# Kernel optimization log

Hardware: AMD Instinct MI355X
Metric: run time of the kernel (lower is better)

Reference implementation:

```python
import jax, jax.numpy as jnp
import numpy as np

PC_RANGE = (-54.0, -54.0, -5.0, 54.0, 54.0, 3.0)
VOXEL = (0.075, 0.075, 0.2)
STRIDE = 8
FW = 180  # feature map size along x
FH = 180  # feature map size along y
NUM_CLASS = 2
M = 500   # num_max_objs
MIN_RADIUS = 2
OVERLAP = 0.1
C_IN = 128
HM_C = 2
REG_C = 9
B = 4


def conv2d(x, w, b=None):
    y = jax.lax.conv_general_dilated(x, w, (1, 1), 'SAME',
                                     dimension_numbers=('NCHW', 'OIHW', 'NCHW'))
    return y if b is None else y + b[None, :, None, None]


def bn(x, g, b, m, v, eps=1e-5):
    inv = g / jnp.sqrt(v + eps)
    return x * inv[None, :, None, None] + (b - m * inv)[None, :, None, None]


def gaussian_radius(height, width, min_overlap):
    # centernet_utils.gaussian_radius
    b1 = height + width
    c1 = width * height * (1.0 - min_overlap) / (1.0 + min_overlap)
    r1 = (b1 + jnp.sqrt(jnp.maximum(b1 * b1 - 4.0 * c1, 0.0))) / 2.0
    b2 = 2.0 * (height + width)
    c2 = (1.0 - min_overlap) * width * height
    r2 = (b2 + jnp.sqrt(jnp.maximum(b2 * b2 - 16.0 * c2, 0.0))) / 2.0
    a3 = 4.0 * min_overlap
    b3 = -2.0 * min_overlap * (height + width)
    c3 = (min_overlap - 1.0) * width * height
    r3 = (b3 + jnp.sqrt(jnp.maximum(b3 * b3 - 4.0 * a3 * c3, 0.0))) / (2.0 * a3)
    return jnp.minimum(jnp.minimum(r1, r2), r3)


def assign_targets(gt):
    # gt: (B, M, 8) = [x, y, z, dx, dy, dz, ry, cls]; cls==0 / zero box = padding
    x, y, z = gt[..., 0], gt[..., 1], gt[..., 2]
    dx, dy, dz, ry = gt[..., 3], gt[..., 4], gt[..., 5], gt[..., 6]
    cls = gt[..., 7].astype(jnp.int32)
    coord_x = jnp.clip((x - PC_RANGE[0]) / VOXEL[0] / STRIDE, 0.0, FW - 0.5)
    coord_y = jnp.clip((y - PC_RANGE[1]) / VOXEL[1] / STRIDE, 0.0, FH - 0.5)
    cxi = coord_x.astype(jnp.int32)
    cyi = coord_y.astype(jnp.int32)
    dxp = dx / VOXEL[0] / STRIDE
    dyp = dy / VOXEL[1] / STRIDE
    radius = jnp.maximum(gaussian_radius(dxp, dyp, OVERLAP).astype(jnp.int32), MIN_RADIUS)
    valid = (dxp > 0) & (dyp > 0)
    pos = valid & (cls >= 1)

    # --- dense gaussian splat, max-reduced per class (= draw_gaussian_to_heatmap) ---
    ddx = jnp.arange(FW)[None, None, :] - cxi[..., None]   # (B,M,FW)
    ddy = jnp.arange(FH)[None, None, :] - cyi[..., None]   # (B,M,FH)
    sigma = (2.0 * radius.astype(jnp.float32) + 1.0) / 6.0
    d2 = (ddy[..., :, None] ** 2 + ddx[..., None, :] ** 2).astype(jnp.float32)  # (B,M,FH,FW)
    g = jnp.exp(-d2 / (2.0 * sigma[..., None, None] ** 2))
    win = (jnp.abs(ddy) <= radius[..., None])[..., :, None] & \
          (jnp.abs(ddx) <= radius[..., None])[..., None, :]
    g = jnp.where(win & pos[..., None, None], g, 0.0)
    seg = jnp.where(pos, cls - 1, NUM_CLASS)
    hmv = jax.vmap(lambda gv, sv: jax.ops.segment_max(gv, sv, num_segments=NUM_CLASS + 1))(
        g.reshape(B, M, FH * FW), seg)
    heatmap = jnp.maximum(hmv[:, :NUM_CLASS].reshape(B, NUM_CLASS, FH, FW), 0.0)
    heatmap_mask = (heatmap > 0).astype(gt.dtype)

    # --- inds / mask / ret_boxes (5 slots per object: center + 4 neighbors) ---
    base_ind = cyi * FW + cxi
    w_cond = VOXEL[0] * STRIDE > dy / 4.0   # faithful: uses temp_w = gt[:,4]
    l_cond = VOXEL[1] * STRIDE > dx / 4.0   # faithful: uses temp_l = gt[:,3]
    left = cxi - 1 >= 0
    right = cxi + 1 < FW
    up = cyi - 1 >= 0
    down = cyi + 1 < FH
    m0 = jnp.where(valid, jnp.where(cls >= 1, 1, -1), 0)
    s1 = valid & ~w_cond & left
    s2 = valid & ~w_cond & right
    s3 = valid & ~l_cond & up
    s4 = valid & ~l_cond & down
    mask = jnp.stack([m0,
                      jnp.where(s1, m0, 0), jnp.where(s2, m0, 0),
                      jnp.where(s3, m0, 0), jnp.where(s4, m0, 0)], -1).reshape(B, 5 * M)
    inds = jnp.stack([jnp.where(valid, base_ind, 0),
                      jnp.where(s1, base_ind - 1, 0), jnp.where(s2, base_ind + 1, 0),
                      jnp.where(s3, base_ind - FW, 0), jnp.where(s4, base_ind + FW, 0)],
                     -1).reshape(B, 5 * M).astype(jnp.int32)
    offx = coord_x - cxi.astype(gt.dtype)
    offy = coord_y - cyi.astype(gt.dtype)
    base = jnp.stack([offx, offy, z,
                      jnp.log(jnp.maximum(dx, 1e-8)),
                      jnp.log(jnp.maximum(dy, 1e-8)),
                      jnp.log(jnp.maximum(dz, 1e-8)),
                      jnp.cos(ry), jnp.sin(ry)], -1)          # (B,M,8)
    z5 = jnp.zeros((B, M), gt.dtype)
    dx_adj = jnp.stack([z5, s1.astype(gt.dtype), -s2.astype(gt.dtype), z5, z5], -1)  # (B,M,5)
    dy_adj = jnp.stack([z5, z5, z5, s3.astype(gt.dtype), -s4.astype(gt.dtype)], -1)
    zero5 = jnp.zeros_like(dx_adj)
    delta = jnp.stack([dx_adj, dy_adj, zero5, zero5, zero5, zero5, zero5, zero5], -1)  # (B,M,5,8)
    rb = (base[:, :, None, :] + delta) * valid[:, :, None, None].astype(gt.dtype)
    ret_boxes = rb.reshape(B, 5 * M, 8)
    return heatmap, ret_boxes, inds, mask, heatmap_mask


def setup_inputs():
    key = jax.random.key(0)
    ks = jax.random.split(key, 12)
    x = jax.random.normal(ks[0], (B, C_IN, FH, FW), jnp.float32)
    # realistic gt boxes; last 150 per scene are zero padding
    cxy = jax.random.uniform(ks[1], (B, M, 2), minval=-50.0, maxval=50.0)
    zc = jax.random.uniform(ks[2], (B, M, 1), minval=-2.0, maxval=1.0)
    dims = jax.random.uniform(ks[3], (B, M, 3), minval=0.5, maxval=6.0)
    ry = jax.random.uniform(ks[4], (B, M, 1), minval=-3.14, maxval=3.14)
    cls = jax.random.randint(ks[5], (B, M, 1), 1, NUM_CLASS + 1).astype(jnp.float32)
    vm = (jnp.arange(M) < 350)[None, :, None].astype(jnp.float32)
    gt_boxes = jnp.concatenate([cxy, zc, dims, ry, cls], -1) * vm
    p = lambda k, s, sc: jax.random.normal(k, s, jnp.float32) * sc
    return {
        'x': x, 'gt_boxes': gt_boxes,
        'conv1_w': p(ks[6], (C_IN, C_IN, 3, 3), 0.02),
        'bn1_g': jnp.ones((C_IN,)), 'bn1_b': jnp.zeros((C_IN,)),
        'bn1_m': jnp.zeros((C_IN,)), 'bn1_v': jnp.ones((C_IN,)),
        'conv2_w': p(ks[7], (C_IN, C_IN, 3, 3), 0.02),
        'bn2_g': jnp.ones((C_IN,)), 'bn2_b': jnp.zeros((C_IN,)),
        'bn2_m': jnp.zeros((C_IN,)), 'bn2_v': jnp.ones((C_IN,)),
        'hm_w': p(ks[8], (HM_C, C_IN, 3, 3), 0.02),
        'hm_b': jnp.full((HM_C,), -2.19, jnp.float32),
        'reg_w': p(ks[9], (REG_C, C_IN, 3, 3), 0.001),
        'reg_b': jnp.zeros((REG_C,), jnp.float32),
    }


def reference(x, gt_boxes, conv1_w, bn1_g, bn1_b, bn1_m, bn1_v,
              conv2_w, bn2_g, bn2_b, bn2_m, bn2_v, hm_w, hm_b, reg_w, reg_b):
    f = jax.nn.relu(bn(conv2d(x, conv1_w), bn1_g, bn1_b, bn1_m, bn1_v))
    f = jax.nn.relu(bn(conv2d(f, conv2_w), bn2_g, bn2_b, bn2_m, bn2_v))
    hm = conv2d(f, hm_w, hm_b)      # (B, 2, H, W)
    reg = conv2d(f, reg_w, reg_b)   # (B, 9, H, W)
    heatmap, ret_boxes, inds, mask, heatmap_mask = assign_targets(gt_boxes)
    return hm, reg, heatmap, ret_boxes, inds, mask, heatmap_mask
```

## Files before the change

### kernel.cpp

```cpp
#include <hip/hip_runtime.h>
#include <math.h>

typedef unsigned short u16;
typedef short bf16x8 __attribute__((ext_vector_type(8)));
typedef float f32x4 __attribute__((ext_vector_type(4)));

#define FW_ 180
#define FH_ 180
#define HW_ (FW_*FH_)
#define CIN_ 128
#define BB_ 4
#define MM_ 500
#define PW_ 182
#define PADE ((size_t)BB_*PW_*PW_*CIN_)

#define HM_OFF   0
#define REG_OFF  (BB_*2*HW_)
#define HEAT_OFF (REG_OFF + BB_*9*HW_)
#define RB_OFF   (HEAT_OFF + BB_*2*HW_)
#define IND_OFF  (RB_OFF + BB_*MM_*5*8)
#define MSK_OFF  (IND_OFF + BB_*MM_*5)
#define HMM_OFF  (MSK_OFF + BB_*MM_*5)

__device__ inline u16 f2bf(float f) {
    unsigned u = __float_as_uint(f);
    u += 0x7FFFu + ((u >> 16) & 1u);
    return (u16)(u >> 16);
}

#define GLOAD_LDS16(gsrc, ldst) \
    __builtin_amdgcn_global_load_lds( \
        (const __attribute__((address_space(1))) unsigned*)(gsrc), \
        (__attribute__((address_space(3))) unsigned*)(ldst), 16, 0, 0)

__global__ void k_init_w(u16* __restrict__ ws, float* __restrict__ out,
                         const float* __restrict__ w1, const float* __restrict__ w2,
                         const float* __restrict__ hw, const float* __restrict__ rw,
                         u16* __restrict__ wT1, u16* __restrict__ wT2,
                         u16* __restrict__ wTh)
{
    int idx = blockIdx.x * 256 + threadIdx.x;
    const int n1 = 3 * BB_ * PW_ * PW_;
    const int n2 = n1 + BB_ * 2 * HW_;
    const int NW = 9 * CIN_ * CIN_;
    const int n3 = n2 + NW;
    const int n4 = n3 + NW;
    const int n5 = n4 + 9 * 16 * CIN_;
    if (idx < n1) {
        int buf = idx / (BB_ * PW_ * PW_);
        int rem = idx % (BB_ * PW_ * PW_);
        int p = rem % (PW_ * PW_);
        int r = p / PW_, c = p % PW_;
        if (r > 0 && r < PW_ - 1 && c > 0 && c < PW_ - 1) return;
        u16* base = ws + (size_t)buf * PADE + (size_t)rem * CIN_;
#pragma unroll
        for (int i = 0; i < 16; ++i) ((uint4*)base)[i] = make_uint4(0, 0, 0, 0);
    } else if (idx < n2) {
        out[HEAT_OFF + (idx - n1)] = 0.f;
    } else if (idx < n3) {
        int j = idx - n2;
        int tap = j / (CIN_ * CIN_);
        int r = j % (CIN_ * CIN_);
        int co = r >> 7, ci = r & 127;
        wT1[j] = f2bf(w1[((size_t)co * CIN_ + ci) * 9 + tap]);
    } else if (idx < n4) {
        int j = idx - n3;
        int tap = j / (CIN_ * CIN_);
        int r = j % (CIN_ * CIN_);
        int co = r >> 7, ci = r & 127;
        wT2[j] = f2bf(w2[((size_t)co * CIN_ + ci) * 9 + tap]);
    } else if (idx < n5) {
        int j = idx - n4;
        int tap = j / (16 * CIN_);
        int r = j % (16 * CIN_);
        int co = r >> 7, ci = r & 127;
        float v = 0.f;
        if (co < 2)       v = hw[((size_t)co * CIN_ + ci) * 9 + tap];
        else if (co < 11) v = rw[((size_t)(co - 2) * CIN_ + ci) * 9 + tap];
        wTh[j] = f2bf(v);
    }
}

__global__ __launch_bounds__(256) void k_prep_xT(const float* __restrict__ in,
                                                 u16* __restrict__ xT)
{
    __shared__ unsigned lt32[180 * 65];
    int tid = threadIdx.x;
    int row = blockIdx.x, b = blockIdx.y;
    const float* inr = in + ((size_t)b * CIN_ * FH_ + row) * FW_;
    for (int i = tid; i < 64 * 45; i += 256) {
        int ci2 = i / 45, c4 = i - 45 * ci2;
        const float* p0 = inr + (size_t)(2 * ci2) * HW_ + c4 * 4;
        float4 a = *(const float4*)p0;
        float4 bq = *(const float4*)(p0 + HW_);
        lt32[(c4 * 4 + 0) * 65 + ci2] = (unsigned)f2bf(a.x) | ((unsigned)f2bf(bq.x) << 16);
        lt32[(c4 * 4 + 1) * 65 + ci2] = (unsigned)f2bf(a.y) | ((unsigned)f2bf(bq.y) << 16);
        lt32[(c4 * 4 + 2) * 65 + ci2] = (unsigned)f2bf(a.z) | ((unsigned)f2bf(bq.z) << 16);
        lt32[(c4 * 4 + 3) * 65 + ci2] = (unsigned)f2bf(a.w) | ((unsigned)f2bf(bq.w) << 16);
    }
    __syncthreads();
    unsigned* dst = (unsigned*)(xT + ((size_t)b * PW_ * PW_ + (size_t)(row + 1) * PW_ + 1) * CIN_);
    for (int idx = tid; idx < 180 * 16; idx += 256) {
        int col = idx >> 4, q = idx & 15;
        uint4 v;
        v.x = lt32[col * 65 + q * 4 + 0];
        v.y = lt32[col * 65 + q * 4 + 1];
        v.z = lt32[col * 65 + q * 4 + 2];
        v.w = lt32[col * 65 + q * 4 + 3];
        *(uint4*)&dst[col * 64 + q * 4] = v;
    }
}

__global__ __launch_bounds__(256, 2) void k_conv_v13(
    const u16* __restrict__ xT, const u16* __restrict__ wT,
    const float* __restrict__ gg, const float* __restrict__ bbn,
    const float* __restrict__ mmn, const float* __restrict__ vvn,
    u16* __restrict__ yT)
{
    __shared__ u16 lin[1600 * 8];
    __shared__ u16 lwt[3][768 * 8];

    int tid  = threadIdx.x;
    int wv   = tid >> 6, lane = tid & 63;
    int lm   = lane & 15, hi = lane >> 4;

    int wg   = blockIdx.x;
    int wgid = (wg & 7) * 135 + (wg >> 3);
    int b    = wgid / 270;
    int rem  = wgid % 270;
    int row  = rem / 6;
    int t6   = rem % 6;
    int csp  = t6 % 3, cog = t6 / 3;
    int C0   = (csp == 2) ? 116 : csp * 64;
    int cob  = cog * 64;
    int R0   = row * 4;
    const u16* xb = xT + (size_t)b * PW_ * PW_ * CIN_;

    f32x4 acc[4][4];
#pragma unroll
    for (int i = 0; i < 4; ++i)
#pragma unroll
        for (int j = 0; j < 4; ++j) acc[i][j] = (f32x4){0.f, 0.f, 0.f, 0.f};

    unsigned soffI[6];
#pragma unroll
    for (int rd = 0; rd < 6; ++rd) {
        int o = rd * 256 + tid;
        int rc = o >> 2;
        int r = rc / 66, c = rc - 66 * r;
        int q = (o & 3) ^ ((c >> 1) & 3);
        soffI[rd] = (unsigned)(((R0 + r) * PW_ + (C0 + c)) * CIN_ + q * 8);
    }
    unsigned soffX = 0;
    if (tid < 64) {
        int o = 1536 + tid;
        int rc = o >> 2;
        int r = rc / 66, c = rc - 66 * r;
        if (o >= 1584) { r = 5; c = 65; }
        int q = (o & 3) ^ ((c >> 1) & 3);
        soffX = (unsigned)(((R0 + r) * PW_ + (C0 + c)) * CIN_ + q * 8);
    }
    const int wco = tid >> 2;
    const int wq  = (tid & 3) ^ ((wco >> 1) & 3);
    const unsigned soffW = (unsigned)((cob + wco) * CIN_ + wq * 8);

    #define STAGE_IN(CH)                                                        \
    {                                                                           \
        _Pragma("unroll")                                                       \
        for (int rd = 0; rd < 6; ++rd)                                          \
            GLOAD_LDS16(xb + soffI[rd] + (CH) * 32,                             \
                        &lin[(size_t)(rd * 256 + wv * 64) * 8]);                \
        if (tid < 64)                                                           \
            GLOAD_LDS16(xb + soffX + (CH) * 32, &lin[(size_t)1536 * 8]);        \
    }
    #define STAGE_W(NCH, NTG)                                                   \
    {                                                                           \
        _Pragma("unroll")                                                       \
        for (int rd = 0; rd < 3; ++rd)                                          \
            GLOAD_LDS16(wT + (size_t)((NTG) * 3 + rd) * CIN_ * CIN_ + soffW + (NCH) * 32, \
                        &lwt[NTG][(size_t)(rd * 256 + wv * 64) * 8]);           \
    }
    #define COMPUTE_TG(TG)                                                      \
    {                                                                           \
        _Pragma("unroll")                                                       \
        for (int t = 0; t < 3; ++t) {                                           \
            bf16x8 av[4];                                                       \
            _Pragma("unroll")                                                   \
            for (int mf = 0; mf < 4; ++mf) {                                    \
                int col = mf * 16 + lm;                                         \
                int unit = t * 256 + col * 4 + (hi ^ ((col >> 1) & 3));         \
                av[mf] = *(const bf16x8*)&lwt[TG][(size_t)unit * 8];            \
            }                                                                   \
            _Pragma("unroll")                                                   \
            for (int nf = 0; nf < 4; ++nf) {                                    \
                int c = wv * 16 + lm + t;                                       \
                int rc = (nf + (TG)) * 66 + c;                                  \
                int unit = rc * 4 + (hi ^ ((c >> 1) & 3));                      \
                bf16x8 bv = *(const bf16x8*)&lin[(size_t)unit * 8];             \
                _Pragma("unroll")                                               \
                for (int mf = 0; mf < 4; ++mf)                                  \
                    acc[mf][nf] = __builtin_amdgcn_mfma_f32_16x16x32_bf16(      \
                        av[mf], bv, acc[mf][nf], 0, 0, 0);                      \
            }                                                                   \
        }                                                                       \
    }

    STAGE_IN(0);
    STAGE_W(0, 0);

#pragma unroll
    for (int ch = 0; ch < 4; ++ch) {
#pragma unroll
        for (int tg = 0; tg < 3; ++tg) {
            if (tg == 0 && ch > 0) {
                __builtin_amdgcn_s_barrier();
                __builtin_amdgcn_sched_barrier(0);
                STAGE_IN(ch);
            }
            const bool last = (ch == 3 && tg == 2);
            if (!last) {
                const int nch = (tg == 2) ? ch + 1 : ch;
                const int ntg = (tg + 1) % 3;
                STAGE_W(nch, ntg);
                asm volatile("s_waitcnt vmcnt(3)" ::: "memory");
            } else {
                asm volatile("s_waitcnt vmcnt(0)" ::: "memory");
            }
            __builtin_amdgcn_s_barrier();
            __builtin_amdgcn_sched_barrier(0);
            COMPUTE_TG(tg);
        }
    }
    #undef STAGE_IN
    #undef STAGE_W
    #undef COMPUTE_TG

#pragma unroll
    for (int mf = 0; mf < 4; ++mf) {
        int co0 = cob + mf * 16 + hi * 4;
        float4 g4 = *(const float4*)(gg + co0);
        float4 b4 = *(const float4*)(bbn + co0);
        float4 m4 = *(const float4*)(mmn + co0);
        float4 v4 = *(const float4*)(vvn + co0);
        float sc0 = g4.x / sqrtf(v4.x + 1e-5f), sh0 = b4.x - m4.x * sc0;
        float sc1 = g4.y / sqrtf(v4.y + 1e-5f), sh1 = b4.y - m4.y * sc1;
        float sc2 = g4.z / sqrtf(v4.z + 1e-5f), sh2 = b4.z - m4.z * sc2;
        float sc3 = g4.w / sqrtf(v4.w + 1e-5f), sh3 = b4.w - m4.w * sc3;
#pragma unroll
        for (int nf = 0; nf < 4; ++nf) {
            f32x4 A = acc[mf][nf];
            float y0 = fmaxf(fmaf(A[0], sc0, sh0), 0.f);
            float y1 = fmaxf(fmaf(A[1], sc1, sh1), 0.f);
            float y2 = fmaxf(fmaf(A[2], sc2, sh2), 0.f);
            float y3 = fmaxf(fmaf(A[3], sc3, sh3), 0.f);
            unsigned p0 = (unsigned)f2bf(y0) | ((unsigned)f2bf(y1) << 16);
            unsigned p1 = (unsigned)f2bf(y2) | ((unsigned)f2bf(y3) << 16);
            u16* op = yT + (size_t)b * PW_ * PW_ * CIN_ +
                      ((size_t)(R0 + nf + 1) * PW_ + (C0 + wv * 16 + lm + 1)) * CIN_ + co0;
            *(uint2*)op = make_uint2(p0, p1);
        }
    }
}

__global__ __launch_bounds__(256) void k_head_v9(
    const u16* __restrict__ f2T, const u16* __restrict__ wTh,
    const float* __restrict__ hb, const float* __restrict__ rb,
    float* __restrict__ out)
{
    __shared__ u16 lin[1600 * 8];
    __shared__ u16 lwt[2304 * 8];

    int tid  = threadIdx.x;
    int wv   = tid >> 6, lane = tid & 63;
    int lm   = lane & 15, hi = lane >> 4;
    int csp  = blockIdx.x;
    int C0   = (csp == 2) ? 116 : csp * 64;
    int R0   = blockIdx.y * 4;
    int b    = blockIdx.z;
    const u16* xb = f2T + (size_t)b * PW_ * PW_ * CIN_;

    f32x4 acc[4];
#pragma unroll
    for (int i = 0; i < 4; ++i) acc[i] = (f32x4){0.f, 0.f, 0.f, 0.f};

#pragma unroll
    for (int rd = 0; rd < 9; ++rd) {
        int o = rd * 256 + tid;
        int tap = o >> 8, rest = o & 255;
        int co = rest >> 4, u8s = rest & 15;
        const u16* src = wTh + (size_t)tap * 16 * CIN_ + co * CIN_ + ((u8s ^ (co & 7)) * 8);
        GLOAD_LDS16(src, &lwt[(size_t)(rd * 256 + wv * 64) * 8]);
    }

#pragma unroll 1
    for (int ch = 0; ch < 4; ++ch) {
        int ci0 = ch * 32;
        __syncthreads();
#pragma unroll
        for (int rd = 0; rd < 6; ++rd) {
            int o = rd * 256 + tid;
            int rc = o >> 2;
            int r = rc / 66, c = rc - 66 * r;
            int q = (o & 3) ^ ((c >> 1) & 3);
            const u16* src = xb + ((size_t)(R0 + r) * PW_ + (C0 + c)) * CIN_ + ci0 + q * 8;
            GLOAD_LDS16(src, &lin[(size_t)(rd * 256 + wv * 64) * 8]);
        }
        if (tid < 64) {
            int o = 1536 + tid;
            int rc = o >> 2;
            int r = rc / 66, c = rc - 66 * r;
            if (o >= 1584) { r = 5; c = 65; }
            int q = (o & 3) ^ ((c >> 1) & 3);
            const u16* src = xb + ((size_t)(R0 + r) * PW_ + (C0 + c)) * CIN_ + ci0 + q * 8;
            GLOAD_LDS16(src, &lin[(size_t)1536 * 8]);
        }
        __syncthreads();

#pragma unroll
        for (int tap = 0; tap < 9; ++tap) {
            const int kr = tap / 3, kc = tap - 3 * (tap / 3);
            int u8 = (ch * 4 + hi) ^ (lm & 7);
            bf16x8 av = *(const bf16x8*)&lwt[(size_t)(tap * 256 + lm * 16 + u8) * 8];
#pragma unroll
            for (int nf = 0; nf < 4; ++nf) {
                int c = wv * 16 + lm + kc;
                int rc = (nf + kr) * 66 + c;
                int unit = rc * 4 + (hi ^ ((c >> 1) & 3));
                bf16x8 bv = *(const bf16x8*)&lin[(size_t)unit * 8];
                acc[nf] = __builtin_amdgcn_mfma_f32_16x16x32_bf16(av, bv, acc[nf], 0, 0, 0);
            }
        }
    }

#pragma unroll
    for (int nf = 0; nf < 4; ++nf) {
        int row = R0 + nf, col = C0 + wv * 16 + lm;
        f32x4 A = acc[nf];
#pragma unroll
        for (int r = 0; r < 4; ++r) {
            int co = hi * 4 + r;
            float v = A[r];
            if (co < 2)
                out[HM_OFF + ((size_t)(b * 2 + co)) * HW_ + (size_t)row * FW_ + col] = v + hb[co];
            else if (co < 11)
                out[REG_OFF + ((size_t)(b * 9 + co - 2)) * HW_ + (size_t)row * FW_ + col] = v + rb[co - 2];
        }
    }

    int blk = (b * 45 + (int)blockIdx.y) * 3 + csp;
    int base = blk * 480;
    for (int i = base + tid; i < base + 480; i += 256) {
        float v = out[HEAT_OFF + i];
        out[HMM_OFF + i] = v > 0.f ? 1.f : 0.f;
    }
}

__global__ void k_objects(const float* __restrict__ gt, float* __restrict__ out)
{
    int ob = blockIdx.x;
    int b = ob / MM_, m = ob % MM_;
    const float* gp = gt + (size_t)ob * 8;
    float x = gp[0], y = gp[1], z = gp[2];
    float dx = gp[3], dy = gp[4], dz = gp[5], ry = gp[6];
    int cls = (int)gp[7];

    float coord_x = fminf(fmaxf((x + 54.f) / 0.075f / 8.f, 0.f), 179.5f);
    float coord_y = fminf(fmaxf((y + 54.f) / 0.075f / 8.f, 0.f), 179.5f);
    int cxi = (int)coord_x, cyi = (int)coord_y;
    float dxp = dx / 0.075f / 8.f;
    float dyp = dy / 0.075f / 8.f;

    float hgt = dxp, wid = dyp, mo = 0.1f;
    float b1 = hgt + wid, c1 = wid * hgt * (1.f - mo) / (1.f + mo);
    float r1 = (b1 + sqrtf(fmaxf(b1 * b1 - 4.f * c1, 0.f))) * 0.5f;
    float b2 = 2.f * (hgt + wid), c2 = (1.f - mo) * wid * hgt;
    float r2 = (b2 + sqrtf(fmaxf(b2 * b2 - 16.f * c2, 0.f))) * 0.5f;
    float a3 = 4.f * mo, b3 = -2.f * mo * (hgt + wid), c3 = (mo - 1.f) * wid * hgt;
    float r3 = (b3 + sqrtf(fmaxf(b3 * b3 - 4.f * a3 * c3, 0.f))) / (2.f * a3);
    int radius = max((int)fminf(fminf(r1, r2), r3), 2);

    bool valid = (dxp > 0.f) && (dyp > 0.f);
    bool pos = valid && (cls >= 1);

    if (threadIdx.x == 0) {
        float m0 = valid ? (cls >= 1 ? 1.f : -1.f) : 0.f;
        bool w_cond = (0.075f * 8.f) > dy / 4.f;
        bool l_cond = (0.075f * 8.f) > dx / 4.f;
        bool s1 = valid && !w_cond && (cxi - 1 >= 0);
        bool s2 = valid && !w_cond && (cxi + 1 < FW_);
        bool s3 = valid && !l_cond && (cyi - 1 >= 0);
        bool s4 = valid && !l_cond && (cyi + 1 < FH_);
        int base_ind = cyi * FW_ + cxi;

        float* indp = out + IND_OFF + (size_t)b * MM_ * 5 + m * 5;
        float* mskp = out + MSK_OFF + (size_t)b * MM_ * 5 + m * 5;
        indp[0] = valid ? (float)base_ind : 0.f;
        indp[1] = s1 ? (float)(base_ind - 1) : 0.f;
        indp[2] = s2 ? (float)(base_ind + 1) : 0.f;
        indp[3] = s3 ? (float)(base_ind - FW_) : 0.f;
        indp[4] = s4 ? (float)(base_ind + FW_) : 0.f;
        mskp[0] = m0;
        mskp[1] = s1 ? m0 : 0.f;
        mskp[2] = s2 ? m0 : 0.f;
        mskp[3] = s3 ? m0 : 0.f;
        mskp[4] = s4 ? m0 : 0.f;

        float offx = coord_x - (float)cxi;
        float offy = coord_y - (float)cyi;
        float bse[8] = { offx, offy, z,
                         logf(fmaxf(dx, 1e-8f)), logf(fmaxf(dy, 1e-8f)),
                         logf(fmaxf(dz, 1e-8f)), cosf(ry), sinf(ry) };
        float vm = valid ? 1.f : 0.f;
        float* rbp = out + RB_OFF + ((size_t)b * MM_ + m) * 5 * 8;
#pragma unroll
        for (int s = 0; s < 5; ++s) {
            float t0 = bse[0], t1 = bse[1];
            if (s == 1) t0 += s1 ? 1.f : 0.f;
            if (s == 2) t0 -= s2 ? 1.f : 0.f;
            if (s == 3) t1 += s3 ? 1.f : 0.f;
            if (s == 4) t1 -= s4 ? 1.f : 0.f;
            rbp[s * 8 + 0] = t0 * vm;
            rbp[s * 8 + 1] = t1 * vm;
#pragma unroll
            for (int k = 2; k < 8; ++k) rbp[s * 8 + k] = bse[k] * vm;
        }
    }

    if (pos) {
        float sigma = (2.f * (float)radius + 1.f) / 6.f;
        float inv2s2 = 1.f / (2.f * sigma * sigma);
        int x0 = max(cxi - radius, 0), x1 = min(cxi + radius, FW_ - 1);
        int y0 = max(cyi - radius, 0), y1 = min(cyi + radius, FH_ - 1);
        int wdt = x1 - x0 + 1, tot = wdt * (y1 - y0 + 1);
        float* hp = out + HEAT_OFF + (size_t)(b * 2 + (cls - 1)) * HW_;
        for (int i = threadIdx.x; i < tot; i += blockDim.x) {
            int yy = y0 + i / wdt, xx = x0 + i % wdt;
            float ddy = (float)(yy - cyi), ddx = (float)(xx - cxi);
            float gvl = expf(-(ddy * ddy + ddx * ddx) * inv2s2);
            atomicMax((int*)(hp + yy * FW_ + xx), __float_as_int(gvl));
        }
    }
}

extern "C" void kernel_launch(void* const* d_in, const int* in_sizes, int n_in,
                              void* d_out, int out_size, void* d_ws, size_t ws_size,
                              hipStream_t stream)
{
    const float* x  = (const float*)d_in[0];
    const float* gt = (const float*)d_in[1];
    const float* w1 = (const float*)d_in[2];
    const float* g1 = (const float*)d_in[3];
    const float* b1 = (const float*)d_in[4];
    const float* m1 = (const float*)d_in[5];
    const float* v1 = (const float*)d_in[6];
    const float* w2 = (const float*)d_in[7];
    const float* g2 = (const float*)d_in[8];
    const float* b2 = (const float*)d_in[9];
    const float* m2 = (const float*)d_in[10];
    const float* v2 = (const float*)d_in[11];
    const float* hw = (const float*)d_in[12];
    const float* hb = (const float*)d_in[13];
    const float* rw = (const float*)d_in[14];
    const float* rb = (const float*)d_in[15];
    float* out = (float*)d_out;

    u16* ws  = (u16*)d_ws;
    u16* xT  = ws;
    u16* f1T = ws + PADE;
    u16* f2T = ws + 2 * PADE;
    u16* wT1 = ws + 3 * PADE;
    u16* wT2 = wT1 + 9 * CIN_ * CIN_;
    u16* wTh = wT2 + 9 * CIN_ * CIN_;

    const int NTOT = 3 * BB_ * PW_ * PW_ + BB_ * 2 * HW_
                   + 2 * 9 * CIN_ * CIN_ + 9 * 16 * CIN_;
    k_init_w<<<(NTOT + 255) / 256, 256, 0, stream>>>(ws, out, w1, w2, hw, rw,
                                                     wT1, wT2, wTh);
    k_prep_xT<<<dim3(180, BB_), 256, 0, stream>>>(x, xT);
    k_objects<<<BB_ * MM_, 64, 0, stream>>>(gt, out);

    k_conv_v13<<<1080, 256, 0, stream>>>(xT,  wT1, g1, b1, m1, v1, f1T);
    k_conv_v13<<<1080, 256, 0, stream>>>(f1T, wT2, g2, b2, m2, v2, f2T);

    dim3 hg(3, 45, BB_);
    k_head_v9<<<hg, 256, 0, stream>>>(f2T, wTh, hb, rb, out);
}
```

Measured before the change: 147.2 us.

## Merge prep kernels and fold object target assignment into first conv launch

Combines weight init, border zeroing, heatmap clear and the input transpose into a single k_pre launch. Border zeroing now enumerates only the 724 pad cells per image instead of scanning every padded pixel. The per-object target work now runs as 500 extra blocks of the first conv launch, one wave per object, which removes the separate k_objects launch and overlaps it with conv work. This cuts launch count and wasted threads, but adds branching to the conv kernel and may disturb its block scheduling.

Result: faster. 137.0 us (median of 3 runs) (-6.9%).

```diff
diff --git a/kernel.cpp b/kernel.cpp
--- a/kernel.cpp
+++ b/kernel.cpp
@@ -33,92 +33,188 @@
         (const __attribute__((address_space(1))) unsigned*)(gsrc), \
         (__attribute__((address_space(3))) unsigned*)(ldst), 16, 0, 0)
 
-__global__ void k_init_w(u16* __restrict__ ws, float* __restrict__ out,
-                         const float* __restrict__ w1, const float* __restrict__ w2,
-                         const float* __restrict__ hw, const float* __restrict__ rw,
-                         u16* __restrict__ wT1, u16* __restrict__ wT2,
-                         u16* __restrict__ wTh)
+__device__ void obj_work(int ob, int lane, const float* __restrict__ gt,
+                         float* __restrict__ out)
 {
-    int idx = blockIdx.x * 256 + threadIdx.x;
-    const int n1 = 3 * BB_ * PW_ * PW_;
-    const int n2 = n1 + BB_ * 2 * HW_;
+    int b = ob / MM_, m = ob % MM_;
+    const float* gp = gt + (size_t)ob * 8;
+    float x = gp[0], y = gp[1], z = gp[2];
+    float dx = gp[3], dy = gp[4], dz = gp[5], ry = gp[6];
+    int cls = (int)gp[7];
+
+    float coord_x = fminf(fmaxf((x + 54.f) / 0.075f / 8.f, 0.f), 179.5f);
+    float coord_y = fminf(fmaxf((y + 54.f) / 0.075f / 8.f, 0.f), 179.5f);
+    int cxi = (int)coord_x, cyi = (int)coord_y;
+    float dxp = dx / 0.075f / 8.f;
+    float dyp = dy / 0.075f / 8.f;
+
+    float hgt = dxp, wid = dyp, mo = 0.1f;
+    float b1 = hgt + wid, c1 = wid * hgt * (1.f - mo) / (1.f + mo);
+    float r1 = (b1 + sqrtf(fmaxf(b1 * b1 - 4.f * c1, 0.f))) * 0.5f;
+    float b2 = 2.f * (hgt + wid), c2 = (1.f - mo) * wid * hgt;
+    float r2 = (b2 + sqrtf(fmaxf(b2 * b2 - 16.f * c2, 0.f))) * 0.5f;
+    float a3 = 4.f * mo, b3 = -2.f * mo * (hgt + wid), c3 = (mo - 1.f) * wid * hgt;
+    float r3 = (b3 + sqrtf(fmaxf(b3 * b3 - 4.f * a3 * c3, 0.f))) / (2.f * a3);
+    int radius = max((int)fminf(fminf(r1, r2), r3), 2);
+
+    bool valid = (dxp > 0.f) && (dyp > 0.f);
+    bool pos = valid && (cls >= 1);
+
+    if (lane == 0) {
+        float m0 = valid ? (cls >= 1 ? 1.f : -1.f) : 0.f;
+        bool w_cond = (0.075f * 8.f) > dy / 4.f;
+        bool l_cond = (0.075f * 8.f) > dx / 4.f;
+        bool s1 = valid && !w_cond && (cxi - 1 >= 0);
+        bool s2 = valid && !w_cond && (cxi + 1 < FW_);
+        bool s3 = valid && !l_cond && (cyi - 1 >= 0);
+        bool s4 = valid && !l_cond && (cyi + 1 < FH_);
+        int base_ind = cyi * FW_ + cxi;
+
+        float* indp = out + IND_OFF + (size_t)b * MM_ * 5 + m * 5;
+        float* mskp = out + MSK_OFF + (size_t)b * MM_ * 5 + m * 5;
+        indp[0] = valid ? (float)base_ind : 0.f;
+        indp[1] = s1 ? (float)(base_ind - 1) : 0.f;
+        indp[2] = s2 ? (float)(base_ind + 1) : 0.f;
+        indp[3] = s3 ? (float)(base_ind - FW_) : 0.f;
+        indp[4] = s4 ? (float)(base_ind + FW_) : 0.f;
+        mskp[0] = m0;
+        mskp[1] = s1 ? m0 : 0.f;
+        mskp[2] = s2 ? m0 : 0.f;
+        mskp[3] = s3 ? m0 : 0.f;
+        mskp[4] = s4 ? m0 : 0.f;
+
+        float offx = coord_x - (float)cxi;
+        float offy = coord_y - (float)cyi;
+        float bse[8] = { offx, offy, z,
+                         logf(fmaxf(dx, 1e-8f)), logf(fmaxf(dy, 1e-8f)),
+                         logf(fmaxf(dz, 1e-8f)), cosf(ry), sinf(ry) };
+        float vm = valid ? 1.f : 0.f;
+        float* rbp = out + RB_OFF + ((size_t)b * MM_ + m) * 5 * 8;
+#pragma unroll
+        for (int s = 0; s < 5; ++s) {
+            float t0 = bse[0], t1 = bse[1];
+            if (s == 1) t0 += s1 ? 1.f : 0.f;
+            if (s == 2) t0 -= s2 ? 1.f : 0.f;
+            if (s == 3) t1 += s3 ? 1.f : 0.f;
+            if (s == 4) t1 -= s4 ? 1.f : 0.f;
+            rbp[s * 8 + 0] = t0 * vm;
+            rbp[s * 8 + 1] = t1 * vm;
+#pragma unroll
+            for (int k = 2; k < 8; ++k) rbp[s * 8 + k] = bse[k] * vm;
+        }
+    }
+
+    if (pos) {
+        float sigma = (2.f * (float)radius + 1.f) / 6.f;
+        float inv2s2 = 1.f / (2.f * sigma * sigma);
+        int x0 = max(cxi - radius, 0), x1 = min(cxi + radius, FW_ - 1);
+        int y0 = max(cyi - radius, 0), y1 = min(cyi + radius, FH_ - 1);
+        int wdt = x1 - x0 + 1, tot = wdt * (y1 - y0 + 1);
+        float* hp = out + HEAT_OFF + (size_t)(b * 2 + (cls - 1)) * HW_;
+        for (int i = lane; i < tot; i += 64) {
+            int yy = y0 + i / wdt, xx = x0 + i % wdt;
+            float ddy = (float)(yy - cyi), ddx = (float)(xx - cxi);
+            float gvl = expf(-(ddy * ddy + ddx * ddx) * inv2s2);
+            atomicMax((int*)(hp + yy * FW_ + xx), __float_as_int(gvl));
+        }
+    }
+}
+
+__global__ __launch_bounds__(256) void k_pre(
+    const float* __restrict__ x, u16* __restrict__ xT, u16* __restrict__ ws,
+    float* __restrict__ out,
+    const float* __restrict__ w1, const float* __restrict__ w2,
+    const float* __restrict__ hw, const float* __restrict__ rw,
+    u16* __restrict__ wT1, u16* __restrict__ wT2, u16* __restrict__ wTh)
+{
+    __shared__ unsigned lt32[180 * 65];
+    int tid = threadIdx.x;
+    if (blockIdx.x < 720) {
+        int row = blockIdx.x % 180, b = blockIdx.x / 180;
+        const float* inr = x + ((size_t)b * CIN_ * FH_ + row) * FW_;
+        for (int i = tid; i < 64 * 45; i += 256) {
+            int ci2 = i / 45, c4 = i - 45 * ci2;
+            const float* p0 = inr + (size_t)(2 * ci2) * HW_ + c4 * 4;
+            float4 a = *(const float4*)p0;
+            float4 bq = *(const float4*)(p0 + HW_);
+            lt32[(c4 * 4 + 0) * 65 + ci2] = (unsigned)f2bf(a.x) | ((unsigned)f2bf(bq.x) << 16);
+            lt32[(c4 * 4 + 1) * 65 + ci2] = (unsigned)f2bf(a.y) | ((unsigned)f2bf(bq.y) << 16);
+            lt32[(c4 * 4 + 2) * 65 + ci2] = (unsigned)f2bf(a.z) | ((unsigned)f2bf(bq.z) << 16);
+            lt32[(c4 * 4 + 3) * 65 + ci2] = (unsigned)f2bf(a.w) | ((unsigned)f2bf(bq.w) << 16);
+        }
+        __syncthreads();
+        unsigned* dst = (unsigned*)(xT + ((size_t)b * PW_ * PW_ + (size_t)(row + 1) * PW_ + 1) * CIN_);
+        for (int idx = tid; idx < 180 * 16; idx += 256) {
+            int col = idx >> 4, q = idx & 15;
+            uint4 v;
+            v.x = lt32[col * 65 + q * 4 + 0];
+            v.y = lt32[col * 65 + q * 4 + 1];
+            v.z = lt32[col * 65 + q * 4 + 2];
+            v.w = lt32[col * 65 + q * 4 + 3];
+            *(uint4*)&dst[col * 64 + q * 4] = v;
+        }
+        return;
+    }
+
+    int idx = (blockIdx.x - 720) * 256 + tid;
+    if (idx < 12 * 724) {
+        int which = idx / 724, cell = idx % 724;
+        int buf = which >> 2, b = which & 3;
+        int r, c;
+        if (cell < 182)      { r = 0;   c = cell; }
+        else if (cell < 364) { r = 181; c = cell - 182; }
+        else { int s = cell - 364; r = 1 + (s >> 1); c = (s & 1) ? 181 : 0; }
+        u16* base = ws + (size_t)buf * PADE + ((size_t)b * PW_ * PW_ + (size_t)r * PW_ + c) * CIN_;
+#pragma unroll
+        for (int i = 0; i < 16; ++i) ((uint4*)base)[i] = make_uint4(0, 0, 0, 0);
+        return;
+    }
+    idx -= 12 * 724;
+    if (idx < BB_ * 2 * HW_) { out[HEAT_OFF + idx] = 0.f; return; }
+    idx -= BB_ * 2 * HW_;
     const int NW = 9 * CIN_ * CIN_;
-    const int n3 = n2 + NW;
-    const int n4 = n3 + NW;
-    const int n5 = n4 + 9 * 16 * CIN_;
-    if (idx < n1) {
-        int buf = idx / (BB_ * PW_ * PW_);
-        int rem = idx % (BB_ * PW_ * PW_);
-        int p = rem % (PW_ * PW_);
-        int r = p / PW_, c = p % PW_;
-        if (r > 0 && r < PW_ - 1 && c > 0 && c < PW_ - 1) return;
-        u16* base = ws + (size_t)buf * PADE + (size_t)rem * CIN_;
-#pragma unroll
-        for (int i = 0; i < 16; ++i) ((uint4*)base)[i] = make_uint4(0, 0, 0, 0);
-    } else if (idx < n2) {
-        out[HEAT_OFF + (idx - n1)] = 0.f;
-    } else if (idx < n3) {
-        int j = idx - n2;
-        int tap = j / (CIN_ * CIN_);
-        int r = j % (CIN_ * CIN_);
+    if (idx < NW) {
+        int tap = idx / (CIN_ * CIN_);
+        int r = idx % (CIN_ * CIN_);
         int co = r >> 7, ci = r & 127;
-        wT1[j] = f2bf(w1[((size_t)co * CIN_ + ci) * 9 + tap]);
-    } else if (idx < n4) {
-        int j = idx - n3;
-        int tap = j / (CIN_ * CIN_);
-        int r = j % (CIN_ * CIN_);
+        wT1[idx] = f2bf(w1[((size_t)co * CIN_ + ci) * 9 + tap]);
+        return;
+    }
+    idx -= NW;
+    if (idx < NW) {
+        int tap = idx / (CIN_ * CIN_);
+        int r = idx % (CIN_ * CIN_);
         int co = r >> 7, ci = r & 127;
-        wT2[j] = f2bf(w2[((size_t)co * CIN_ + ci) * 9 + tap]);
-    } else if (idx < n5) {
-        int j = idx - n4;
-        int tap = j / (16 * CIN_);
-        int r = j % (16 * CIN_);
+        wT2[idx] = f2bf(w2[((size_t)co * CIN_ + ci) * 9 + tap]);
+        return;
+    }
+    idx -= NW;
+    if (idx < 9 * 16 * CIN_) {
+        int tap = idx / (16 * CIN_);
+        int r = idx % (16 * CIN_);
         int co = r >> 7, ci = r & 127;
         float v = 0.f;
         if (co < 2)       v = hw[((size_t)co * CIN_ + ci) * 9 + tap];
         else if (co < 11) v = rw[((size_t)(co - 2) * CIN_ + ci) * 9 + tap];
-        wTh[j] = f2bf(v);
-    }
-}
-
-__global__ __launch_bounds__(256) void k_prep_xT(const float* __restrict__ in,
-                                                 u16* __restrict__ xT)
-{
-    __shared__ unsigned lt32[180 * 65];
-    int tid = threadIdx.x;
-    int row = blockIdx.x, b = blockIdx.y;
-    const float* inr = in + ((size_t)b * CIN_ * FH_ + row) * FW_;
-    for (int i = tid; i < 64 * 45; i += 256) {
-        int ci2 = i / 45, c4 = i - 45 * ci2;
-        const float* p0 = inr + (size_t)(2 * ci2) * HW_ + c4 * 4;
-        float4 a = *(const float4*)p0;
-        float4 bq = *(const float4*)(p0 + HW_);
-        lt32[(c4 * 4 + 0) * 65 + ci2] = (unsigned)f2bf(a.x) | ((unsigned)f2bf(bq.x) << 16);
-        lt32[(c4 * 4 + 1) * 65 + ci2] = (unsigned)f2bf(a.y) | ((unsigned)f2bf(bq.y) << 16);
-        lt32[(c4 * 4 + 2) * 65 + ci2] = (unsigned)f2bf(a.z) | ((unsigned)f2bf(bq.z) << 16);
-        lt32[(c4 * 4 + 3) * 65 + ci2] = (unsigned)f2bf(a.w) | ((unsigned)f2bf(bq.w) << 16);
-    }
-    __syncthreads();
-    unsigned* dst = (unsigned*)(xT + ((size_t)b * PW_ * PW_ + (size_t)(row + 1) * PW_ + 1) * CIN_);
-    for (int idx = tid; idx < 180 * 16; idx += 256) {
-        int col = idx >> 4, q = idx & 15;
-        uint4 v;
-        v.x = lt32[col * 65 + q * 4 + 0];
-        v.y = lt32[col * 65 + q * 4 + 1];
-        v.z = lt32[col * 65 + q * 4 + 2];
-        v.w = lt32[col * 65 + q * 4 + 3];
-        *(uint4*)&dst[col * 64 + q * 4] = v;
-    }
-}
-
-__global__ __launch_bounds__(256, 2) void k_conv_v13(
+        wTh[idx] = f2bf(v);
+    }
+}
+
+__global__ __launch_bounds__(256, 2) void k_conv_v15(
     const u16* __restrict__ xT, const u16* __restrict__ wT,
     const float* __restrict__ gg, const float* __restrict__ bbn,
     const float* __restrict__ mmn, const float* __restrict__ vvn,
-    u16* __restrict__ yT)
+    u16* __restrict__ yT,
+    const float* __restrict__ gt, float* __restrict__ outp)
 {
     __shared__ u16 lin[1600 * 8];
     __shared__ u16 lwt[3][768 * 8];
+
+    if (blockIdx.x >= 1080) {
+        int ob = ((int)blockIdx.x - 1080) * 4 + ((int)threadIdx.x >> 6);
+        obj_work(ob, threadIdx.x & 63, gt, outp);
+        return;
+    }
 
     int tid  = threadIdx.x;
     int wv   = tid >> 6, lane = tid & 63;
@@ -355,93 +451,6 @@
     }
 }
 
-__global__ void k_objects(const float* __restrict__ gt, float* __restrict__ out)
-{
-    int ob = blockIdx.x;
-    int b = ob / MM_, m = ob % MM_;
-    const float* gp = gt + (size_t)ob * 8;
-    float x = gp[0], y = gp[1], z = gp[2];
-    float dx = gp[3], dy = gp[4], dz = gp[5], ry = gp[6];
-    int cls = (int)gp[7];
-
-    float coord_x = fminf(fmaxf((x + 54.f) / 0.075f / 8.f, 0.f), 179.5f);
-    float coord_y = fminf(fmaxf((y + 54.f) / 0.075f / 8.f, 0.f), 179.5f);
-    int cxi = (int)coord_x, cyi = (int)coord_y;
-    float dxp = dx / 0.075f / 8.f;
-    float dyp = dy / 0.075f / 8.f;
-
-    float hgt = dxp, wid = dyp, mo = 0.1f;
-    float b1 = hgt + wid, c1 = wid * hgt * (1.f - mo) / (1.f + mo);
-    float r1 = (b1 + sqrtf(fmaxf(b1 * b1 - 4.f * c1, 0.f))) * 0.5f;
-    float b2 = 2.f * (hgt + wid), c2 = (1.f - mo) * wid * hgt;
-    float r2 = (b2 + sqrtf(fmaxf(b2 * b2 - 16.f * c2, 0.f))) * 0.5f;
-    float a3 = 4.f * mo, b3 = -2.f * mo * (hgt + wid), c3 = (mo - 1.f) * wid * hgt;
-    float r3 = (b3 + sqrtf(fmaxf(b3 * b3 - 4.f * a3 * c3, 0.f))) / (2.f * a3);
-    int radius = max((int)fminf(fminf(r1, r2), r3), 2);
-
-    bool valid = (dxp > 0.f) && (dyp > 0.f);
-    bool pos = valid && (cls >= 1);
-
-    if (threadIdx.x == 0) {
-        float m0 = valid ? (cls >= 1 ? 1.f : -1.f) : 0.f;
-        bool w_cond = (0.075f * 8.f) > dy / 4.f;
-        bool l_cond = (0.075f * 8.f) > dx / 4.f;
-        bool s1 = valid && !w_cond && (cxi - 1 >= 0);
-        bool s2 = valid && !w_cond && (cxi + 1 < FW_);
-        bool s3 = valid && !l_cond && (cyi - 1 >= 0);
-        bool s4 = valid && !l_cond && (cyi + 1 < FH_);
-        int base_ind = cyi * FW_ + cxi;
-
-        float* indp = out + IND_OFF + (size_t)b * MM_ * 5 + m * 5;
-        float* mskp = out + MSK_OFF + (size_t)b * MM_ * 5 + m * 5;
-        indp[0] = valid ? (float)base_ind : 0.f;
-        indp[1] = s1 ? (float)(base_ind - 1) : 0.f;
-        indp[2] = s2 ? (float)(base_ind + 1) : 0.f;
-        indp[3] = s3 ? (float)(base_ind - FW_) : 0.f;
-        indp[4] = s4 ? (float)(base_ind + FW_) : 0.f;
-        mskp[0] = m0;
-        mskp[1] = s1 ? m0 : 0.f;
-        mskp[2] = s2 ? m0 : 0.f;
-        mskp[3] = s3 ? m0 : 0.f;
-        mskp[4] = s4 ? m0 : 0.f;
-
-        float offx = coord_x - (float)cxi;
-        float offy = coord_y - (float)cyi;
-        float bse[8] = { offx, offy, z,
-                         logf(fmaxf(dx, 1e-8f)), logf(fmaxf(dy, 1e-8f)),
-                         logf(fmaxf(dz, 1e-8f)), cosf(ry), sinf(ry) };
-        float vm = valid ? 1.f : 0.f;
-        float* rbp = out + RB_OFF + ((size_t)b * MM_ + m) * 5 * 8;
-#pragma unroll
-        for (int s = 0; s < 5; ++s) {
-            float t0 = bse[0], t1 = bse[1];
-            if (s == 1) t0 += s1 ? 1.f : 0.f;
-            if (s == 2) t0 -= s2 ? 1.f : 0.f;
-            if (s == 3) t1 += s3 ? 1.f : 0.f;
-            if (s == 4) t1 -= s4 ? 1.f : 0.f;
-            rbp[s * 8 + 0] = t0 * vm;
-            rbp[s * 8 + 1] = t1 * vm;
-#pragma unroll
-            for (int k = 2; k < 8; ++k) rbp[s * 8 + k] = bse[k] * vm;
-        }
-    }
-
-    if (pos) {
-        float sigma = (2.f * (float)radius + 1.f) / 6.f;
-        float inv2s2 = 1.f / (2.f * sigma * sigma);
-        int x0 = max(cxi - radius, 0), x1 = min(cxi + radius, FW_ - 1);
-        int y0 = max(cyi - radius, 0), y1 = min(cyi + radius, FH_ - 1);
-        int wdt = x1 - x0 + 1, tot = wdt * (y1 - y0 + 1);
-        float* hp = out + HEAT_OFF + (size_t)(b * 2 + (cls - 1)) * HW_;
-        for (int i = threadIdx.x; i < tot; i += blockDim.x) {
-            int yy = y0 + i / wdt, xx = x0 + i % wdt;
-            float ddy = (float)(yy - cyi), ddx = (float)(xx - cxi);
-            float gvl = expf(-(ddy * ddy + ddx * ddx) * inv2s2);
-            atomicMax((int*)(hp + yy * FW_ + xx), __float_as_int(gvl));
-        }
-    }
-}
-
 extern "C" void kernel_launch(void* const* d_in, const int* in_sizes, int n_in,
                               void* d_out, int out_size, void* d_ws, size_t ws_size,
                               hipStream_t stream)
@@ -472,15 +481,12 @@
     u16* wT2 = wT1 + 9 * CIN_ * CIN_;
     u16* wTh = wT2 + 9 * CIN_ * CIN_;
 
-    const int NTOT = 3 * BB_ * PW_ * PW_ + BB_ * 2 * HW_
-                   + 2 * 9 * CIN_ * CIN_ + 9 * 16 * CIN_;
-    k_init_w<<<(NTOT + 255) / 256, 256, 0, stream>>>(ws, out, w1, w2, hw, rw,
-                                                     wT1, wT2, wTh);
-    k_prep_xT<<<dim3(180, BB_), 256, 0, stream>>>(x, xT);
-    k_objects<<<BB_ * MM_, 64, 0, stream>>>(gt, out);
-
-    k_conv_v13<<<1080, 256, 0, stream>>>(xT,  wT1, g1, b1, m1, v1, f1T);
-    k_conv_v13<<<1080, 256, 0, stream>>>(f1T, wT2, g2, b2, m2, v2, f2T);
+    const int NFLAT = 12 * 724 + BB_ * 2 * HW_ + 2 * 9 * CIN_ * CIN_ + 9 * 16 * CIN_;
+    const int NPRE  = 720 + (NFLAT + 255) / 256;
+    k_pre<<<NPRE, 256, 0, stream>>>(x, xT, ws, out, w1, w2, hw, rw, wT1, wT2, wTh);
+
+    k_conv_v15<<<1080 + 500, 256, 0, stream>>>(xT,  wT1, g1, b1, m1, v1, f1T, gt, out);
+    k_conv_v15<<<1080,       256, 0, stream>>>(f1T, wT2, g2, b2, m2, v2, f2T, gt, out);
 
     dim3 hg(3, 45, BB_);
     k_head_v9<<<hg, 256, 0, stream>>>(f2T, wTh, hb, rb, out);
```
